# Kernel optimization log

Measured on AMD Instinct MI355X. Metric: run time of the kernel, lower is better.

## Reference

```python
import jax, jax.numpy as jnp
import numpy as np

NEG_INF = -1e9

def setup_inputs() -> dict:
    key = jax.random.key(0)
    ks = jax.random.split(key, 6)
    B, M, RNN, H, D = 64, 1024, 1024, 512, 2048
    return {
        "h": jax.random.normal(ks[0], (B, RNN), dtype=jnp.float32),
        "att_feats": jax.random.normal(ks[1], (B, M, D), dtype=jnp.float32),
        "att_mask": jax.random.randint(ks[2], (B, M), 0, 2, dtype=jnp.int32),
        "p_att_feats": jax.random.normal(ks[3], (B, M, H), dtype=jnp.float32),
        "W_ah": jax.random.normal(ks[4], (H, RNN), dtype=jnp.float32) * (1.0 / np.sqrt(RNN)),
        "w_alpha": jax.random.normal(ks[5], (H,), dtype=jnp.float32) * (1.0 / np.sqrt(H)),
    }

def reference(h, att_feats, att_mask, p_att_feats, W_ah, w_alpha):
    # Wah(h): [B, H]
    wah = h @ W_ah.T
    # additive attention energies: tanh(Wah(h)[:, None, :] + p_att_feats) -> [B, M, H]
    e = jnp.tanh(wah[:, None, :] + p_att_feats)
    # project to scalar per region: [B, M]
    logits = jnp.einsum("bmh,h->bm", e, w_alpha)
    logits = jnp.where(att_mask == 0, NEG_INF, logits)
    alpha = jax.nn.softmax(logits, axis=-1)
    # weighted sum of region features: [B, D]
    att = jnp.einsum("bm,bmd->bd", alpha, att_feats)
    return att
```

## Files before the change

### kernel.cpp

```cpp
#include <hip/hip_runtime.h>
#include <math.h>

#define B   64
#define M   1024
#define RNN 1024
#define H   512
#define D   2048
#define NEG_INF -1e9f

#define MBLK   8
#define MCHUNK (M / MBLK)

__device__ __forceinline__ float fast_tanh(float x) {
    float ax = fabsf(x);
    float t  = __expf(-2.0f * ax);
    float r  = (1.0f - t) / (1.0f + t);
    return copysignf(r, x);
}

__global__ __launch_bounds__(256) void k_wah(const float* __restrict__ h,
                                             const float* __restrict__ W,
                                             float* __restrict__ wah) {
    int wid  = (blockIdx.x * 256 + threadIdx.x) >> 6;
    int lane = threadIdx.x & 63;
    int b = wid >> 9;
    int j = wid & (H - 1);
    const float4* hp = (const float4*)(h + (size_t)b * RNN);
    const float4* wp = (const float4*)(W + (size_t)j * RNN);
    float acc = 0.0f;
#pragma unroll
    for (int t = 0; t < 4; ++t) {
        int i = lane + t * 64;
        float4 a = hp[i];
        float4 w = wp[i];
        acc += a.x * w.x + a.y * w.y + a.z * w.z + a.w * w.w;
    }
#pragma unroll
    for (int off = 32; off > 0; off >>= 1)
        acc += __shfl_down(acc, off);
    if (lane == 0) wah[wid] = acc;
}

__global__ __launch_bounds__(256) void k_logits(const float* __restrict__ wah,
                                                const float* __restrict__ p_att,
                                                const int* __restrict__ mask,
                                                const float* __restrict__ w_alpha,
                                                float* __restrict__ logits) {
    int row  = (blockIdx.x * 256 + threadIdx.x) >> 6;
    int lane = threadIdx.x & 63;
    int b = row >> 10;
    if (mask[row] == 0) {
        if (lane == 0) logits[row] = NEG_INF;
        return;
    }
    const float4* pp  = (const float4*)(p_att + (size_t)row * H);
    const float4* whp = (const float4*)(wah + (size_t)b * H);
    const float4* wap = (const float4*)w_alpha;
    float acc = 0.0f;
#pragma unroll
    for (int t = 0; t < 2; ++t) {
        int i = lane + t * 64;
        float4 p  = pp[i];
        float4 wh = whp[i];
        float4 wa = wap[i];
        acc += fast_tanh(p.x + wh.x) * wa.x;
        acc += fast_tanh(p.y + wh.y) * wa.y;
        acc += fast_tanh(p.z + wh.z) * wa.z;
        acc += fast_tanh(p.w + wh.w) * wa.w;
    }
#pragma unroll
    for (int off = 32; off > 0; off >>= 1)
        acc += __shfl_down(acc, off);
    if (lane == 0) logits[row] = acc;
}

__global__ __launch_bounds__(64) void k_softmax(const float* __restrict__ logits,
                                                float* __restrict__ alpha) {
    int b    = blockIdx.x;
    int lane = threadIdx.x;
    const float4* lg = (const float4*)(logits + (size_t)b * M);
    float4 v[4];
    float mx = -INFINITY;
#pragma unroll
    for (int t = 0; t < 4; ++t) {
        v[t] = lg[lane + t * 64];
        mx = fmaxf(mx, fmaxf(fmaxf(v[t].x, v[t].y), fmaxf(v[t].z, v[t].w)));
    }
#pragma unroll
    for (int off = 32; off > 0; off >>= 1)
        mx = fmaxf(mx, __shfl_xor(mx, off));
    float sum = 0.0f;
#pragma unroll
    for (int t = 0; t < 4; ++t) {
        v[t].x = __expf(v[t].x - mx);
        v[t].y = __expf(v[t].y - mx);
        v[t].z = __expf(v[t].z - mx);
        v[t].w = __expf(v[t].w - mx);
        sum += v[t].x + v[t].y + v[t].z + v[t].w;
    }
#pragma unroll
    for (int off = 32; off > 0; off >>= 1)
        sum += __shfl_xor(sum, off);
    float inv = 1.0f / sum;
    float4* ap = (float4*)(alpha + (size_t)b * M);
#pragma unroll
    for (int t = 0; t < 4; ++t) {
        float4 o;
        o.x = v[t].x * inv; o.y = v[t].y * inv;
        o.z = v[t].z * inv; o.w = v[t].w * inv;
        ap[lane + t * 64] = o;
    }
}

__global__ __launch_bounds__(256) void k_att_partial(const float* __restrict__ alpha,
                                                     const float* __restrict__ feats,
                                                     float* __restrict__ partial) {
    int b    = blockIdx.x;
    int dblk = blockIdx.y;
    int mblk = blockIdx.z;
    int d0   = dblk * 1024 + threadIdx.x * 4;

    __shared__ float sa[MCHUNK];
    const float* al = alpha + (size_t)b * M + (size_t)mblk * MCHUNK;
    if (threadIdx.x < MCHUNK) sa[threadIdx.x] = al[threadIdx.x];
    __syncthreads();

    const float4* fp = (const float4*)(feats + ((size_t)b * M + (size_t)mblk * MCHUNK) * D + d0);
    float4 acc = {0.f, 0.f, 0.f, 0.f};
    for (int m = 0; m < MCHUNK; ++m) {
        float a = sa[m];
        if (a != 0.0f) {
            float4 f = fp[(size_t)m * (D / 4)];
            acc.x += a * f.x; acc.y += a * f.y;
            acc.z += a * f.z; acc.w += a * f.w;
        }
    }
    float4* op = (float4*)(partial + ((size_t)mblk * B + b) * D + d0);
    *op = acc;
}

__global__ __launch_bounds__(256) void k_att_reduce(const float* __restrict__ partial,
                                                    float* __restrict__ out) {
    int i = blockIdx.x * 256 + threadIdx.x;
    float s = 0.0f;
#pragma unroll
    for (int mb = 0; mb < MBLK; ++mb)
        s += partial[(size_t)mb * (B * D) + i];
    out[i] = s;
}

extern "C" void kernel_launch(void* const* d_in, const int* in_sizes, int n_in,
                              void* d_out, int out_size, void* d_ws, size_t ws_size,
                              hipStream_t stream) {
    const float* h       = (const float*)d_in[0];
    const float* feats   = (const float*)d_in[1];
    const int*   mask    = (const int*)d_in[2];
    const float* p_att   = (const float*)d_in[3];
    const float* W_ah    = (const float*)d_in[4];
    const float* w_alpha = (const float*)d_in[5];
    float* out = (float*)d_out;

    float* ws      = (float*)d_ws;
    float* wah     = ws;
    float* logits  = wah + B * H;
    float* alpha   = logits + B * M;
    float* partial = alpha + B * M;

    k_wah        <<<dim3(B * H / 4), 256, 0, stream>>>(h, W_ah, wah);
    k_logits     <<<dim3(B * M / 4), 256, 0, stream>>>(wah, p_att, mask, w_alpha, logits);
    k_softmax    <<<dim3(B), 64, 0, stream>>>(logits, alpha);
    k_att_partial<<<dim3(B, D / 1024, MBLK), 256, 0, stream>>>(alpha, feats, partial);
    k_att_reduce <<<dim3(B * D / 256), 256, 0, stream>>>(partial, out);
}
```

Before: 94.10 us.

## Fuse softmax into weighted-sum kernel and compact nonzero alpha indices

Removes the separate softmax launch: each att_partial block recomputes the row max and sum from the logits and derives its own chunk of alpha values. It then compacts the nonzero alpha entries into a shared-memory index list via ballot/popcount, so the feature loop runs branch-free over only the unmasked rows, unrolled by four. This saves one kernel launch and the alpha round trip through memory, and gives more independent loads per iteration. The cost is redundant softmax work in every block (16 blocks per batch row) and extra barriers.

```diff
diff --git a/kernel.cpp b/kernel.cpp
--- a/kernel.cpp
+++ b/kernel.cpp
@@ -74,69 +74,82 @@
     if (lane == 0) logits[row] = acc;
 }
 
-__global__ __launch_bounds__(64) void k_softmax(const float* __restrict__ logits,
-                                                float* __restrict__ alpha) {
-    int b    = blockIdx.x;
-    int lane = threadIdx.x;
+__global__ __launch_bounds__(256) void k_att_partial(const float* __restrict__ logits,
+                                                     const float* __restrict__ feats,
+                                                     float* __restrict__ partial) {
+    const int b    = blockIdx.x;
+    const int dblk = blockIdx.y;
+    const int mblk = blockIdx.z;
+    const int tid  = threadIdx.x;
+    const int lane = tid & 63;
+    const int wid  = tid >> 6;
+
+    __shared__ float s_logit[M];
+    __shared__ float s_red[4];
+    __shared__ float s_a[MCHUNK];
+    __shared__ unsigned short s_idx[MCHUNK];
+    __shared__ int s_c0, s_cnt;
+
     const float4* lg = (const float4*)(logits + (size_t)b * M);
-    float4 v[4];
-    float mx = -INFINITY;
-#pragma unroll
-    for (int t = 0; t < 4; ++t) {
-        v[t] = lg[lane + t * 64];
-        mx = fmaxf(mx, fmaxf(fmaxf(v[t].x, v[t].y), fmaxf(v[t].z, v[t].w)));
-    }
+    float4 v = lg[tid];
+    ((float4*)s_logit)[tid] = v;
+    float mx = fmaxf(fmaxf(v.x, v.y), fmaxf(v.z, v.w));
 #pragma unroll
     for (int off = 32; off > 0; off >>= 1)
         mx = fmaxf(mx, __shfl_xor(mx, off));
-    float sum = 0.0f;
-#pragma unroll
-    for (int t = 0; t < 4; ++t) {
-        v[t].x = __expf(v[t].x - mx);
-        v[t].y = __expf(v[t].y - mx);
-        v[t].z = __expf(v[t].z - mx);
-        v[t].w = __expf(v[t].w - mx);
-        sum += v[t].x + v[t].y + v[t].z + v[t].w;
-    }
+    if (lane == 0) s_red[wid] = mx;
+    __syncthreads();
+    mx = fmaxf(fmaxf(s_red[0], s_red[1]), fmaxf(s_red[2], s_red[3]));
+
+    float se = __expf(v.x - mx) + __expf(v.y - mx) + __expf(v.z - mx) + __expf(v.w - mx);
 #pragma unroll
     for (int off = 32; off > 0; off >>= 1)
-        sum += __shfl_xor(sum, off);
-    float inv = 1.0f / sum;
-    float4* ap = (float4*)(alpha + (size_t)b * M);
-#pragma unroll
-    for (int t = 0; t < 4; ++t) {
-        float4 o;
-        o.x = v[t].x * inv; o.y = v[t].y * inv;
-        o.z = v[t].z * inv; o.w = v[t].w * inv;
-        ap[lane + t * 64] = o;
+        se += __shfl_xor(se, off);
+    __syncthreads();
+    if (lane == 0) s_red[wid] = se;
+    __syncthreads();
+    const float inv = 1.0f / (s_red[0] + s_red[1] + s_red[2] + s_red[3]);
+
+    float a = 0.0f;
+    bool pred = false;
+    if (tid < MCHUNK) {
+        a = __expf(s_logit[mblk * MCHUNK + tid] - mx) * inv;
+        pred = (a != 0.0f);
     }
-}
+    unsigned long long bal = __ballot(pred);
+    int pos = __popcll(bal & ((1ull << lane) - 1ull));
+    if (wid == 0 && lane == 0) s_c0 = __popcll(bal);
+    if (wid == 0 && pred) { s_idx[pos] = (unsigned short)tid; s_a[pos] = a; }
+    __syncthreads();
+    const int c0 = s_c0;
+    if (wid == 1 && pred) { s_idx[c0 + pos] = (unsigned short)(tid & 127); s_a[c0 + pos] = a; }
+    if (wid == 1 && lane == 0) s_cnt = c0 + __popcll(bal);
+    __syncthreads();
+    const int cnt = s_cnt;
 
-__global__ __launch_bounds__(256) void k_att_partial(const float* __restrict__ alpha,
-                                                     const float* __restrict__ feats,
-                                                     float* __restrict__ partial) {
-    int b    = blockIdx.x;
-    int dblk = blockIdx.y;
-    int mblk = blockIdx.z;
-    int d0   = dblk * 1024 + threadIdx.x * 4;
-
-    __shared__ float sa[MCHUNK];
-    const float* al = alpha + (size_t)b * M + (size_t)mblk * MCHUNK;
-    if (threadIdx.x < MCHUNK) sa[threadIdx.x] = al[threadIdx.x];
-    __syncthreads();
-
-    const float4* fp = (const float4*)(feats + ((size_t)b * M + (size_t)mblk * MCHUNK) * D + d0);
+    const int d0 = dblk * 1024 + tid * 4;
+    const float* fbase = feats + ((size_t)b * M + (size_t)mblk * MCHUNK) * D + d0;
     float4 acc = {0.f, 0.f, 0.f, 0.f};
-    for (int m = 0; m < MCHUNK; ++m) {
-        float a = sa[m];
-        if (a != 0.0f) {
-            float4 f = fp[(size_t)m * (D / 4)];
-            acc.x += a * f.x; acc.y += a * f.y;
-            acc.z += a * f.z; acc.w += a * f.w;
-        }
+    int i = 0;
+    for (; i + 4 <= cnt; i += 4) {
+        int m0 = s_idx[i], m1 = s_idx[i + 1], m2 = s_idx[i + 2], m3 = s_idx[i + 3];
+        float a0 = s_a[i], a1 = s_a[i + 1], a2 = s_a[i + 2], a3 = s_a[i + 3];
+        float4 f0 = *(const float4*)(fbase + (size_t)m0 * D);
+        float4 f1 = *(const float4*)(fbase + (size_t)m1 * D);
+        float4 f2 = *(const float4*)(fbase + (size_t)m2 * D);
+        float4 f3 = *(const float4*)(fbase + (size_t)m3 * D);
+        acc.x += a0 * f0.x; acc.y += a0 * f0.y; acc.z += a0 * f0.z; acc.w += a0 * f0.w;
+        acc.x += a1 * f1.x; acc.y += a1 * f1.y; acc.z += a1 * f1.z; acc.w += a1 * f1.w;
+        acc.x += a2 * f2.x; acc.y += a2 * f2.y; acc.z += a2 * f2.z; acc.w += a2 * f2.w;
+        acc.x += a3 * f3.x; acc.y += a3 * f3.y; acc.z += a3 * f3.z; acc.w += a3 * f3.w;
     }
-    float4* op = (float4*)(partial + ((size_t)mblk * B + b) * D + d0);
-    *op = acc;
+    for (; i < cnt; ++i) {
+        int m0 = s_idx[i];
+        float a0 = s_a[i];
+        float4 f0 = *(const float4*)(fbase + (size_t)m0 * D);
+        acc.x += a0 * f0.x; acc.y += a0 * f0.y; acc.z += a0 * f0.z; acc.w += a0 * f0.w;
+    }
+    *(float4*)(partial + ((size_t)mblk * B + b) * D + d0) = acc;
 }
 
 __global__ __launch_bounds__(256) void k_att_reduce(const float* __restrict__ partial,
@@ -163,12 +176,10 @@
     float* ws      = (float*)d_ws;
     float* wah     = ws;
     float* logits  = wah + B * H;
-    float* alpha   = logits + B * M;
-    float* partial = alpha + B * M;
+    float* partial = logits + B * M;
 
     k_wah        <<<dim3(B * H / 4), 256, 0, stream>>>(h, W_ah, wah);
     k_logits     <<<dim3(B * M / 4), 256, 0, stream>>>(wah, p_att, mask, w_alpha, logits);
-    k_softmax    <<<dim3(B), 64, 0, stream>>>(logits, alpha);
-    k_att_partial<<<dim3(B, D / 1024, MBLK), 256, 0, stream>>>(alpha, feats, partial);
+    k_att_partial<<<dim3(B, D / 1024, MBLK), 256, 0, stream>>>(logits, feats, partial);
     k_att_reduce <<<dim3(B * D / 256), 256, 0, stream>>>(partial, out);
 }
```

Result: faster. 82.18 us (-12.7%).

## Fuse logits, unnormalized softmax and weighted feature sum into one chunked kernel

Applied to the files above, without the earlier changes.

Merges the logits, softmax and partial attention-sum kernels into one kernel per (batch, 64-row chunk). It computes exp(logit) without max subtraction, compacts the unmasked rows into a shared index list, and gathers only those feature rows. Normalization is deferred to the reduce kernel, which sums per-chunk Z partials. This drops the launches and round trips for logits and alpha, but relies on logits being small enough that skipping the max shift cannot overflow exp. The grid also shrinks to 1024 blocks with a serial per-wave row loop.

```diff
diff --git a/kernel.cpp b/kernel.cpp
--- a/kernel.cpp
+++ b/kernel.cpp
@@ -6,15 +6,15 @@
 #define RNN 1024
 #define H   512
 #define D   2048
-#define NEG_INF -1e9f
 
-#define MBLK   8
-#define MCHUNK (M / MBLK)
+#define NCHUNK 16
+#define CROWS  (M / NCHUNK)
+#define RPW    (CROWS / 4)
 
 __device__ __forceinline__ float fast_tanh(float x) {
     float ax = fabsf(x);
     float t  = __expf(-2.0f * ax);
-    float r  = (1.0f - t) / (1.0f + t);
+    float r  = (1.0f - t) * __builtin_amdgcn_rcpf(1.0f + t);
     return copysignf(r, x);
 }
 
@@ -41,112 +41,124 @@
     if (lane == 0) wah[wid] = acc;
 }
 
-__global__ __launch_bounds__(256) void k_logits(const float* __restrict__ wah,
-                                                const float* __restrict__ p_att,
-                                                const int* __restrict__ mask,
-                                                const float* __restrict__ w_alpha,
-                                                float* __restrict__ logits) {
-    int row  = (blockIdx.x * 256 + threadIdx.x) >> 6;
-    int lane = threadIdx.x & 63;
-    int b = row >> 10;
-    if (mask[row] == 0) {
-        if (lane == 0) logits[row] = NEG_INF;
-        return;
+__global__ __launch_bounds__(256) void k_fused(const float* __restrict__ wah,
+                                               const float* __restrict__ p_att,
+                                               const int* __restrict__ mask,
+                                               const float* __restrict__ w_alpha,
+                                               const float* __restrict__ feats,
+                                               float* __restrict__ partial,
+                                               float* __restrict__ zpart) {
+    const int b   = blockIdx.x;
+    const int c   = blockIdx.y;
+    const int tid = threadIdx.x;
+    const int lane = tid & 63;
+    const int w    = tid >> 6;
+
+    __shared__ float          s_w[CROWS];
+    __shared__ float          s_zred[4];
+    __shared__ unsigned short s_idx[CROWS + 4];
+    __shared__ float          s_val[CROWS + 4];
+    __shared__ int            s_cnt;
+
+    const float4* wh4 = (const float4*)(wah + (size_t)b * H);
+    const float4* wa4 = (const float4*)w_alpha;
+    float4 wh0 = wh4[lane], wh1 = wh4[lane + 64];
+    float4 wa0 = wa4[lane], wa1 = wa4[lane + 64];
+
+    const int   m0   = c * CROWS;
+    const int*  mrow = mask + (size_t)b * M + m0;
+    const float4* pb4 = (const float4*)(p_att + ((size_t)b * M + m0) * H);
+
+    float zsum = 0.0f;
+    for (int r = w * RPW; r < w * RPW + RPW; ++r) {
+        float e = 0.0f;
+        if (mrow[r] != 0) {
+            float4 p0 = pb4[(size_t)r * (H / 4) + lane];
+            float4 p1 = pb4[(size_t)r * (H / 4) + 64 + lane];
+            float s = fast_tanh(p0.x + wh0.x) * wa0.x
+                    + fast_tanh(p0.y + wh0.y) * wa0.y
+                    + fast_tanh(p0.z + wh0.z) * wa0.z
+                    + fast_tanh(p0.w + wh0.w) * wa0.w
+                    + fast_tanh(p1.x + wh1.x) * wa1.x
+                    + fast_tanh(p1.y + wh1.y) * wa1.y
+                    + fast_tanh(p1.z + wh1.z) * wa1.z
+                    + fast_tanh(p1.w + wh1.w) * wa1.w;
+#pragma unroll
+            for (int off = 32; off > 0; off >>= 1)
+                s += __shfl_xor(s, off);
+            e = __expf(s);
+        }
+        if (lane == 0) s_w[r] = e;
+        zsum += e;
     }
-    const float4* pp  = (const float4*)(p_att + (size_t)row * H);
-    const float4* whp = (const float4*)(wah + (size_t)b * H);
-    const float4* wap = (const float4*)w_alpha;
-    float acc = 0.0f;
-#pragma unroll
-    for (int t = 0; t < 2; ++t) {
-        int i = lane + t * 64;
-        float4 p  = pp[i];
-        float4 wh = whp[i];
-        float4 wa = wap[i];
-        acc += fast_tanh(p.x + wh.x) * wa.x;
-        acc += fast_tanh(p.y + wh.y) * wa.y;
-        acc += fast_tanh(p.z + wh.z) * wa.z;
-        acc += fast_tanh(p.w + wh.w) * wa.w;
+    if (lane == 0) s_zred[w] = zsum;
+    __syncthreads();
+    if (tid == 0)
+        zpart[(size_t)c * B + b] = (s_zred[0] + s_zred[1]) + (s_zred[2] + s_zred[3]);
+
+    if (tid < CROWS) {
+        float a = s_w[tid];
+        bool pred = (a != 0.0f);
+        unsigned long long bal = __ballot(pred);
+        int pos = __popcll(bal & ((1ull << lane) - 1ull));
+        if (pred) { s_idx[pos] = (unsigned short)tid; s_val[pos] = a; }
+        int cnt  = __popcll(bal);
+        int npad = (cnt + 3) & ~3;
+        if (lane < npad - cnt) { s_idx[cnt + lane] = 0; s_val[cnt + lane] = 0.0f; }
+        if (lane == 0) s_cnt = npad;
     }
-#pragma unroll
-    for (int off = 32; off > 0; off >>= 1)
-        acc += __shfl_down(acc, off);
-    if (lane == 0) logits[row] = acc;
+    __syncthreads();
+    const int n = s_cnt;
+
+    const float4* fb4 = (const float4*)(feats + ((size_t)b * M + m0) * D)
+                        + (size_t)w * 128 + lane;
+    float4 acc0 = {0.f, 0.f, 0.f, 0.f}, acc1 = {0.f, 0.f, 0.f, 0.f};
+    for (int i = 0; i < n; i += 4) {
+        int   r0 = s_idx[i],     r1 = s_idx[i + 1];
+        int   r2 = s_idx[i + 2], r3 = s_idx[i + 3];
+        float v0 = s_val[i],     v1 = s_val[i + 1];
+        float v2 = s_val[i + 2], v3 = s_val[i + 3];
+        const float4* q0 = fb4 + (size_t)r0 * (D / 4);
+        const float4* q1 = fb4 + (size_t)r1 * (D / 4);
+        const float4* q2 = fb4 + (size_t)r2 * (D / 4);
+        const float4* q3 = fb4 + (size_t)r3 * (D / 4);
+        float4 f00 = q0[0], f01 = q0[64];
+        float4 f10 = q1[0], f11 = q1[64];
+        float4 f20 = q2[0], f21 = q2[64];
+        float4 f30 = q3[0], f31 = q3[64];
+        acc0.x += v0 * f00.x; acc0.y += v0 * f00.y; acc0.z += v0 * f00.z; acc0.w += v0 * f00.w;
+        acc1.x += v0 * f01.x; acc1.y += v0 * f01.y; acc1.z += v0 * f01.z; acc1.w += v0 * f01.w;
+        acc0.x += v1 * f10.x; acc0.y += v1 * f10.y; acc0.z += v1 * f10.z; acc0.w += v1 * f10.w;
+        acc1.x += v1 * f11.x; acc1.y += v1 * f11.y; acc1.z += v1 * f11.z; acc1.w += v1 * f11.w;
+        acc0.x += v2 * f20.x; acc0.y += v2 * f20.y; acc0.z += v2 * f20.z; acc0.w += v2 * f20.w;
+        acc1.x += v2 * f21.x; acc1.y += v2 * f21.y; acc1.z += v2 * f21.z; acc1.w += v2 * f21.w;
+        acc0.x += v3 * f30.x; acc0.y += v3 * f30.y; acc0.z += v3 * f30.z; acc0.w += v3 * f30.w;
+        acc1.x += v3 * f31.x; acc1.y += v3 * f31.y; acc1.z += v3 * f31.z; acc1.w += v3 * f31.w;
+    }
+    float4* ob = (float4*)(partial + ((size_t)c * B + b) * D) + (size_t)w * 128 + lane;
+    ob[0]  = acc0;
+    ob[64] = acc1;
 }
 
-__global__ __launch_bounds__(64) void k_softmax(const float* __restrict__ logits,
-                                                float* __restrict__ alpha) {
-    int b    = blockIdx.x;
-    int lane = threadIdx.x;
-    const float4* lg = (const float4*)(logits + (size_t)b * M);
-    float4 v[4];
-    float mx = -INFINITY;
+__global__ __launch_bounds__(256) void k_reduce(const float* __restrict__ partial,
+                                                const float* __restrict__ zpart,
+                                                float* __restrict__ out) {
+    int i4 = blockIdx.x * 256 + threadIdx.x;
+    int b  = i4 >> 9;
+    float Z = 0.0f;
 #pragma unroll
-    for (int t = 0; t < 4; ++t) {
-        v[t] = lg[lane + t * 64];
-        mx = fmaxf(mx, fmaxf(fmaxf(v[t].x, v[t].y), fmaxf(v[t].z, v[t].w)));
+    for (int c = 0; c < NCHUNK; ++c)
+        Z += zpart[c * B + b];
+    const float4* p4 = (const float4*)partial;
+    float4 s = p4[i4];
+#pragma unroll
+    for (int c = 1; c < NCHUNK; ++c) {
+        float4 v = p4[(size_t)c * (B * D / 4) + i4];
+        s.x += v.x; s.y += v.y; s.z += v.z; s.w += v.w;
     }
-#pragma unroll
-    for (int off = 32; off > 0; off >>= 1)
-        mx = fmaxf(mx, __shfl_xor(mx, off));
-    float sum = 0.0f;
-#pragma unroll
-    for (int t = 0; t < 4; ++t) {
-        v[t].x = __expf(v[t].x - mx);
-        v[t].y = __expf(v[t].y - mx);
-        v[t].z = __expf(v[t].z - mx);
-        v[t].w = __expf(v[t].w - mx);
-        sum += v[t].x + v[t].y + v[t].z + v[t].w;
-    }
-#pragma unroll
-    for (int off = 32; off > 0; off >>= 1)
-        sum += __shfl_xor(sum, off);
-    float inv = 1.0f / sum;
-    float4* ap = (float4*)(alpha + (size_t)b * M);
-#pragma unroll
-    for (int t = 0; t < 4; ++t) {
-        float4 o;
-        o.x = v[t].x * inv; o.y = v[t].y * inv;
-        o.z = v[t].z * inv; o.w = v[t].w * inv;
-        ap[lane + t * 64] = o;
-    }
-}
-
-__global__ __launch_bounds__(256) void k_att_partial(const float* __restrict__ alpha,
-                                                     const float* __restrict__ feats,
-                                                     float* __restrict__ partial) {
-    int b    = blockIdx.x;
-    int dblk = blockIdx.y;
-    int mblk = blockIdx.z;
-    int d0   = dblk * 1024 + threadIdx.x * 4;
-
-    __shared__ float sa[MCHUNK];
-    const float* al = alpha + (size_t)b * M + (size_t)mblk * MCHUNK;
-    if (threadIdx.x < MCHUNK) sa[threadIdx.x] = al[threadIdx.x];
-    __syncthreads();
-
-    const float4* fp = (const float4*)(feats + ((size_t)b * M + (size_t)mblk * MCHUNK) * D + d0);
-    float4 acc = {0.f, 0.f, 0.f, 0.f};
-    for (int m = 0; m < MCHUNK; ++m) {
-        float a = sa[m];
-        if (a != 0.0f) {
-            float4 f = fp[(size_t)m * (D / 4)];
-            acc.x += a * f.x; acc.y += a * f.y;
-            acc.z += a * f.z; acc.w += a * f.w;
-        }
-    }
-    float4* op = (float4*)(partial + ((size_t)mblk * B + b) * D + d0);
-    *op = acc;
-}
-
-__global__ __launch_bounds__(256) void k_att_reduce(const float* __restrict__ partial,
-                                                    float* __restrict__ out) {
-    int i = blockIdx.x * 256 + threadIdx.x;
-    float s = 0.0f;
-#pragma unroll
-    for (int mb = 0; mb < MBLK; ++mb)
-        s += partial[(size_t)mb * (B * D) + i];
-    out[i] = s;
+    float inv = 1.0f / Z;
+    float4 r = {s.x * inv, s.y * inv, s.z * inv, s.w * inv};
+    ((float4*)out)[i4] = r;
 }
 
 extern "C" void kernel_launch(void* const* d_in, const int* in_sizes, int n_in,
@@ -162,13 +174,11 @@
 
     float* ws      = (float*)d_ws;
     float* wah     = ws;
-    float* logits  = wah + B * H;
-    float* alpha   = logits + B * M;
-    float* partial = alpha + B * M;
+    float* zpart   = wah + B * H;
+    float* partial = zpart + NCHUNK * B;
 
-    k_wah        <<<dim3(B * H / 4), 256, 0, stream>>>(h, W_ah, wah);
-    k_logits     <<<dim3(B * M / 4), 256, 0, stream>>>(wah, p_att, mask, w_alpha, logits);
-    k_softmax    <<<dim3(B), 64, 0, stream>>>(logits, alpha);
-    k_att_partial<<<dim3(B, D / 1024, MBLK), 256, 0, stream>>>(alpha, feats, partial);
-    k_att_reduce <<<dim3(B * D / 256), 256, 0, stream>>>(partial, out);
+    k_wah   <<<dim3(B * H / 4), 256, 0, stream>>>(h, W_ah, wah);
+    k_fused <<<dim3(B, NCHUNK), 256, 0, stream>>>(wah, p_att, mask, w_alpha, feats,
+                                                  partial, zpart);
+    k_reduce<<<dim3(B * D / 1024), 256, 0, stream>>>(partial, zpart, out);
 }
```

Result: faster. 80.52 us (-14.4%).
